# Kernel tuning notes

Measured on AMD Instinct MI355X. Metric: run time of the kernel, lower is better.

Reference implementation:

```python
import jax, jax.numpy as jnp
import numpy as np

N_NODES = 100000
N_EDGES = 1600000
D = 128
BN_EPS = 1e-5

def setup_inputs() -> dict:
    key = jax.random.key(0)
    ks = jax.random.split(key, 6)
    h = jax.random.normal(ks[0], (N_NODES, D), dtype=jnp.float32)
    src = jax.random.randint(ks[1], (N_EDGES,), 0, N_NODES, dtype=jnp.int32)
    dst = jax.random.randint(ks[2], (N_EDGES,), 0, N_NODES, dtype=jnp.int32)
    eps = jnp.zeros((1,), dtype=jnp.float32)
    # 2-layer GIN apply_func MLP, scaled for stable activations
    W1 = jax.random.normal(ks[3], (D, D), dtype=jnp.float32) / np.sqrt(D)
    b1 = jnp.zeros((D,), dtype=jnp.float32)
    W2 = jax.random.normal(ks[4], (D, D), dtype=jnp.float32) / np.sqrt(D)
    b2 = jnp.zeros((D,), dtype=jnp.float32)
    gamma = jnp.ones((D,), dtype=jnp.float32)
    beta = jnp.zeros((D,), dtype=jnp.float32)
    return {"h": h, "src": src, "dst": dst, "eps": eps,
            "W1": W1, "b1": b1, "W2": W2, "b2": b2,
            "gamma": gamma, "beta": beta}

def reference(h, src, dst, eps, W1, b1, W2, b2, gamma, beta):
    # --- neighbor sum aggregation: update_all(copy_u('h'), fn.sum) ---
    msgs = h[src]                                   # [E, D] irregular gather
    neigh = jax.ops.segment_sum(msgs, dst, num_segments=N_NODES)  # [N, D]
    # --- eps-scaled self term ---
    x = (1.0 + eps[0]) * h + neigh                  # [N, D]
    # --- apply_func: 2-layer MLP ---
    x = jax.nn.relu(x @ W1 + b1)
    x = x @ W2 + b2
    # --- BatchNorm1d over node dim (training-mode batch stats) ---
    mean = jnp.mean(x, axis=0)
    var = jnp.mean(jnp.square(x - mean), axis=0)
    x = (x - mean) * jax.lax.rsqrt(var + BN_EPS) * gamma + beta
    # --- activation + residual ---
    x = jax.nn.relu(x)
    x = h + x  # residual (in_dim == out_dim)
    return x
```

## Files before the change

### kernel.cpp

```cpp
#include <hip/hip_runtime.h>

#define NN 100000
#define NE 1600000
#define DD 128
#define BN_EPS 1e-5f

#define WSH 6
#define WSZ 64
#define NWIN ((NN + WSZ - 1) / WSZ)
#define NWINP 2048
#define EPB 8192
#define NBLK ((NE + EPB - 1) / EPB)
#define CAP 1536
#define PREPBLKS 828
#define GRID_PS (NBLK + PREPBLKS)
#define BN_BLOCKS 1024

typedef __attribute__((ext_vector_type(8))) short short8;
typedef __attribute__((ext_vector_type(4))) float floatx4;

__device__ __forceinline__ unsigned short f2bf(float f) {
    union { float f; unsigned u; } v; v.f = f;
    return (unsigned short)((v.u + 0x7FFFu + ((v.u >> 16) & 1u)) >> 16);
}
__device__ __forceinline__ float bf2f(unsigned short u) {
    union { unsigned u; float f; } v; v.u = ((unsigned)u) << 16;
    return v.f;
}

__global__ __launch_bounds__(256) void prep_scatter_kernel(
    float* __restrict__ stats,
    const float* __restrict__ W1, const float* __restrict__ W2,
    unsigned short* __restrict__ W1t, unsigned short* __restrict__ W2t,
    const float* __restrict__ h, unsigned short* __restrict__ hb, int do_hb,
    const int* __restrict__ src, const int* __restrict__ dst,
    int* __restrict__ wcnt, int* __restrict__ estage)
{
    __shared__ int lofs[NWINP];
    __shared__ int lcur[NWINP];
    __shared__ int gbase[NWINP];
    __shared__ int sorted[EPB];
    __shared__ int stmp[256];
    int t = threadIdx.x;

    if (blockIdx.x < NBLK) {
        int blk = blockIdx.x;
        for (int w = t; w < NWINP; w += 256) lcur[w] = 0;
        __syncthreads();
        int base = blk * EPB;
        int cnt = min(EPB, NE - base);
        for (int i = t; i < cnt; i += 256)
            atomicAdd(&lcur[dst[base + i] >> WSH], 1);
        __syncthreads();

        int w0 = t * 8;
        int c[8];
        int tsum = 0;
#pragma unroll
        for (int j = 0; j < 8; ++j) { c[j] = lcur[w0 + j]; tsum += c[j]; }
        stmp[t] = tsum;
        __syncthreads();
#pragma unroll
        for (int ofs = 1; ofs < 256; ofs <<= 1) {
            int u = (t >= ofs) ? stmp[t - ofs] : 0;
            __syncthreads();
            stmp[t] += u;
            __syncthreads();
        }
        int excl = stmp[t] - tsum;
#pragma unroll
        for (int j = 0; j < 8; ++j) {
            int w = w0 + j;
            lofs[w] = excl;
            lcur[w] = excl;
            int gb = (w < NWIN && c[j]) ? atomicAdd(&wcnt[w], c[j]) : 0;
            gbase[w] = w * CAP + gb;
            excl += c[j];
        }
        __syncthreads();

        for (int i = t; i < cnt; i += 256) {
            int d = dst[base + i];
            int s = src[base + i];
            int p = atomicAdd(&lcur[d >> WSH], 1);
            sorted[p] = (s << WSH) | (d & (WSZ - 1));
        }
        __syncthreads();

        for (int w = t; w < NWIN; w += 256) {
            int lb = lofs[w], le = lcur[w];
            int g = gbase[w];
            for (int j = lb; j < le; ++j)
                estage[g + (j - lb)] = sorted[j];
        }
    } else {
        int tid0 = (blockIdx.x - NBLK) * 256 + t;
        int stride = PREPBLKS * 256;
        if (tid0 < 2 * DD) stats[tid0] = 0.0f;
        for (int i = tid0; i < DD * DD; i += stride) {
            int n = i >> 7, k = i & 127;
            W1t[i] = f2bf(W1[k * DD + n]);
            W2t[i] = f2bf(W2[k * DD + n]);
        }
        if (do_hb) {
            const float4* h4 = (const float4*)h;
            ushort4* hb4 = (ushort4*)hb;
            for (int i = tid0; i < NN * (DD / 4); i += stride) {
                float4 v = h4[i];
                ushort4 o;
                o.x = f2bf(v.x); o.y = f2bf(v.y); o.z = f2bf(v.z); o.w = f2bf(v.w);
                hb4[i] = o;
            }
        }
    }
}

template <bool HB>
__global__ __launch_bounds__(256) void permgather_mlp_kernel(
    const float* __restrict__ h, const unsigned short* __restrict__ hb,
    const float* __restrict__ eps, const int* __restrict__ wcnt,
    const int* __restrict__ estage,
    const unsigned short* __restrict__ W1t, const unsigned short* __restrict__ W2t,
    const float* __restrict__ b1, const float* __restrict__ b2,
    unsigned short* __restrict__ Y, float* __restrict__ stats)
{
    __shared__ __align__(16) unsigned short xl[WSZ * 136];
    __shared__ __align__(16) char un[17408];

    int* es   = (int*)un;
    int* cnt  = (int*)(un + 6144);
    int* beg  = (int*)(un + 6144 + 256);
    int* cur  = (int*)(un + 6144 + 512);
    int* dh   = (int*)(un + 6144 + 768);
    int* dcur = (int*)(un + 6144 + 1024);
    unsigned char* order = (unsigned char*)(un + 6144 + 1280);
    unsigned short* wl = (unsigned short*)un;
    float* sred = (float*)un;
    float* qred = sred + 2048;

    const int b = blockIdx.x;
    const int t = threadIdx.x;
    const int lane = t & 63;
    const int wv = t >> 6;
    const int m = lane & 15;
    const int hi = lane >> 4;

    if (t < 64) { cnt[t] = 0; dh[t] = 0; }
    __syncthreads();
    int n = min(wcnt[b], CAP);
    int wbase = b * CAP;
    for (int i = t; i < n; i += 256)
        atomicAdd(&cnt[estage[wbase + i] & (WSZ - 1)], 1);
    __syncthreads();
    if (t < 64) beg[t] = cnt[t];
    __syncthreads();
#pragma unroll
    for (int ofs = 1; ofs < 64; ofs <<= 1) {
        int u = (t < 64 && t >= ofs) ? beg[t - ofs] : 0;
        __syncthreads();
        if (t < 64) beg[t] += u;
        __syncthreads();
    }
    if (t < 64) {
        int ex = beg[t] - cnt[t];
        beg[t] = ex;
        cur[t] = ex;
        atomicAdd(&dh[min(cnt[t], 63)], 1);
    }
    __syncthreads();
    if (t < 64) dcur[t] = dh[t];
    __syncthreads();
#pragma unroll
    for (int ofs = 1; ofs < 64; ofs <<= 1) {
        int u = (t < 64 && t >= ofs) ? dcur[t - ofs] : 0;
        __syncthreads();
        if (t < 64) dcur[t] += u;
        __syncthreads();
    }
    if (t < 64) dcur[t] -= dh[t];
    __syncthreads();
    if (t < 64) {
        int p = atomicAdd(&dcur[min(cnt[t], 63)], 1);
        order[p] = (unsigned char)t;
    }
    __syncthreads();
    for (int i = t; i < n; i += 256) {
        int e = estage[wbase + i];
        int p = atomicAdd(&cur[e & (WSZ - 1)], 1);
        es[p] = e >> WSH;
    }
    __syncthreads();

    const float sE = 1.0f + eps[0];
    const float4* h4 = (const float4*)h;
    const short8* hb8 = (const short8*)hb;
    const int c8 = t & 15;
#pragma unroll
    for (int pass = 0; pass < 4; ++pass) {
        int nl = order[pass * 16 + (t >> 4)];
        int node = b * WSZ + nl;
        if (node >= NN) {
            short8 z = {0, 0, 0, 0, 0, 0, 0, 0};
            *(short8*)&xl[nl * 136 + c8 * 8] = z;
            continue;
        }
        float4 a0 = h4[node * 32 + c8 * 2];
        float4 a1 = h4[node * 32 + c8 * 2 + 1];
        float acc[8] = {sE * a0.x, sE * a0.y, sE * a0.z, sE * a0.w,
                        sE * a1.x, sE * a1.y, sE * a1.z, sE * a1.w};
        int e = beg[nl], eend = beg[nl] + cnt[nl];
        if (HB) {
            for (; e + 3 < eend; e += 4) {
                int s0 = es[e], s1 = es[e + 1], s2 = es[e + 2], s3 = es[e + 3];
                short8 v0 = hb8[s0 * 16 + c8];
                short8 v1 = hb8[s1 * 16 + c8];
                short8 v2 = hb8[s2 * 16 + c8];
                short8 v3 = hb8[s3 * 16 + c8];
#pragma unroll
                for (int j = 0; j < 8; ++j) {
                    float t0 = bf2f((unsigned short)v0[j]) + bf2f((unsigned short)v1[j]);
                    float t1 = bf2f((unsigned short)v2[j]) + bf2f((unsigned short)v3[j]);
                    acc[j] += t0 + t1;
                }
            }
            for (; e < eend; ++e) {
                short8 v0 = hb8[es[e] * 16 + c8];
#pragma unroll
                for (int j = 0; j < 8; ++j) acc[j] += bf2f((unsigned short)v0[j]);
            }
        } else {
            for (; e + 1 < eend; e += 2) {
                int s0 = es[e], s1 = es[e + 1];
                float4 u0 = h4[s0 * 32 + c8 * 2], u1 = h4[s0 * 32 + c8 * 2 + 1];
                float4 w0 = h4[s1 * 32 + c8 * 2], w1 = h4[s1 * 32 + c8 * 2 + 1];
                acc[0] += u0.x + w0.x; acc[1] += u0.y + w0.y;
                acc[2] += u0.z + w0.z; acc[3] += u0.w + w0.w;
                acc[4] += u1.x + w1.x; acc[5] += u1.y + w1.y;
                acc[6] += u1.z + w1.z; acc[7] += u1.w + w1.w;
            }
            if (e < eend) {
                int s0 = es[e];
                float4 u0 = h4[s0 * 32 + c8 * 2], u1 = h4[s0 * 32 + c8 * 2 + 1];
                acc[0] += u0.x; acc[1] += u0.y; acc[2] += u0.z; acc[3] += u0.w;
                acc[4] += u1.x; acc[5] += u1.y; acc[6] += u1.z; acc[7] += u1.w;
            }
        }
        short8 o;
#pragma unroll
        for (int j = 0; j < 8; ++j) o[j] = (short)f2bf(acc[j]);
        *(short8*)&xl[nl * 136 + c8 * 8] = o;
    }
    __syncthreads();

    floatx4 acc[8];
#pragma unroll
    for (int i = 0; i < 8; ++i) acc[i] = (floatx4){0.f, 0.f, 0.f, 0.f};
    const short8* W1t8 = (const short8*)W1t;
#pragma unroll
    for (int hh = 0; hh < 2; ++hh) {
#pragma unroll
        for (int l = 0; l < 4; ++l) {
            int idx = t + l * 256;
            int nr = idx >> 4, c = idx & 15;
            *(short8*)&wl[nr * 136 + c * 8] = W1t8[(hh * 64 + nr) * 16 + c];
        }
        __syncthreads();
#pragma unroll
        for (int kc = 0; kc < 4; ++kc) {
            short8 a = *(const short8*)&xl[(wv * 16 + m) * 136 + kc * 32 + hi * 8];
#pragma unroll
            for (int ntl = 0; ntl < 4; ++ntl) {
                short8 bb = *(const short8*)&wl[(ntl * 16 + m) * 136 + kc * 32 + hi * 8];
                acc[hh * 4 + ntl] =
                    __builtin_amdgcn_mfma_f32_16x16x32_bf16(a, bb, acc[hh * 4 + ntl], 0, 0, 0);
            }
        }
        __syncthreads();
    }
#pragma unroll
    for (int nt = 0; nt < 8; ++nt) {
        float bv = b1[nt * 16 + m];
#pragma unroll
        for (int r = 0; r < 4; ++r) {
            float v = fmaxf(acc[nt][r] + bv, 0.f);
            xl[(wv * 16 + hi * 4 + r) * 136 + nt * 16 + m] = f2bf(v);
        }
    }
    __syncthreads();

#pragma unroll
    for (int i = 0; i < 8; ++i) acc[i] = (floatx4){0.f, 0.f, 0.f, 0.f};
    const short8* W2t8 = (const short8*)W2t;
#pragma unroll
    for (int hh = 0; hh < 2; ++hh) {
#pragma unroll
        for (int l = 0; l < 4; ++l) {
            int idx = t + l * 256;
            int nr = idx >> 4, c = idx & 15;
            *(short8*)&wl[nr * 136 + c * 8] = W2t8[(hh * 64 + nr) * 16 + c];
        }
        __syncthreads();
#pragma unroll
        for (int kc = 0; kc < 4; ++kc) {
            short8 a = *(const short8*)&xl[(wv * 16 + m) * 136 + kc * 32 + hi * 8];
#pragma unroll
            for (int ntl = 0; ntl < 4; ++ntl) {
                short8 bb = *(const short8*)&wl[(ntl * 16 + m) * 136 + kc * 32 + hi * 8];
                acc[hh * 4 + ntl] =
                    __builtin_amdgcn_mfma_f32_16x16x32_bf16(a, bb, acc[hh * 4 + ntl], 0, 0, 0);
            }
        }
        __syncthreads();
    }

#pragma unroll
    for (int nt = 0; nt < 8; ++nt) {
        float bv = b2[nt * 16 + m];
        float ss = 0.f, qq = 0.f;
#pragma unroll
        for (int r = 0; r < 4; ++r) {
            int row = wv * 16 + hi * 4 + r;
            float v = acc[nt][r] + bv;
            xl[row * 136 + nt * 16 + m] = f2bf(v);
            if (b * WSZ + row < NN) { ss += v; qq += v * v; }
        }
        sred[(nt * 16 + m) * 16 + wv * 4 + hi] = ss;
        qred[(nt * 16 + m) * 16 + wv * 4 + hi] = qq;
    }
    __syncthreads();

#pragma unroll
    for (int l = 0; l < 4; ++l) {
        int idx = t + l * 256;
        int row = idx >> 4, c = idx & 15;
        int g = b * WSZ + row;
        if (g < NN)
            ((short8*)Y)[g * 16 + c] = *(const short8*)&xl[row * 136 + c * 8];
    }
    if (t < 128) {
        float s = 0.f, q = 0.f;
#pragma unroll
        for (int j = 0; j < 16; ++j) { s += sred[t * 16 + j]; q += qred[t * 16 + j]; }
        atomicAdd(&stats[t], s);
        atomicAdd(&stats[DD + t], q);
    }
}

__global__ __launch_bounds__(256) void bn_final_kernel(
    const unsigned short* __restrict__ Y, const float* __restrict__ h,
    const float* __restrict__ gamma, const float* __restrict__ beta,
    const float* __restrict__ stats, float* __restrict__ out)
{
    const float invN = 1.0f / (float)NN;
    int t0 = blockIdx.x * 256 + threadIdx.x;
    int c8 = t0 & 15;
    float sc[8], sh[8];
#pragma unroll
    for (int j = 0; j < 8; ++j) {
        int col = c8 * 8 + j;
        float mu = stats[col] * invN;
        float var = stats[DD + col] * invN - mu * mu;
        float s = rsqrtf(var + BN_EPS) * gamma[col];
        sc[j] = s;
        sh[j] = beta[col] - mu * s;
    }
    const short8* Y8 = (const short8*)Y;
    const float4* H4 = (const float4*)h;
    float4* O4 = (float4*)out;
    const int total = NN * 16;
    const int stride = BN_BLOCKS * 256;
    for (int i = t0; i < total; i += stride) {
        short8 u = Y8[i];
        float4 h0 = H4[2 * i], h1 = H4[2 * i + 1];
        float4 r0, r1;
        r0.x = h0.x + fmaxf(bf2f((unsigned short)u[0]) * sc[0] + sh[0], 0.f);
        r0.y = h0.y + fmaxf(bf2f((unsigned short)u[1]) * sc[1] + sh[1], 0.f);
        r0.z = h0.z + fmaxf(bf2f((unsigned short)u[2]) * sc[2] + sh[2], 0.f);
        r0.w = h0.w + fmaxf(bf2f((unsigned short)u[3]) * sc[3] + sh[3], 0.f);
        r1.x = h1.x + fmaxf(bf2f((unsigned short)u[4]) * sc[4] + sh[4], 0.f);
        r1.y = h1.y + fmaxf(bf2f((unsigned short)u[5]) * sc[5] + sh[5], 0.f);
        r1.z = h1.z + fmaxf(bf2f((unsigned short)u[6]) * sc[6] + sh[6], 0.f);
        r1.w = h1.w + fmaxf(bf2f((unsigned short)u[7]) * sc[7] + sh[7], 0.f);
        O4[2 * i] = r0;
        O4[2 * i + 1] = r1;
    }
}

extern "C" void kernel_launch(void* const* d_in, const int* in_sizes, int n_in,
                              void* d_out, int out_size, void* d_ws, size_t ws_size,
                              hipStream_t stream)
{
    const float* h     = (const float*)d_in[0];
    const int*   src   = (const int*)d_in[1];
    const int*   dst   = (const int*)d_in[2];
    const float* eps   = (const float*)d_in[3];
    const float* W1    = (const float*)d_in[4];
    const float* b1    = (const float*)d_in[5];
    const float* W2    = (const float*)d_in[6];
    const float* b2    = (const float*)d_in[7];
    const float* gamma = (const float*)d_in[8];
    const float* beta  = (const float*)d_in[9];
    float* out = (float*)d_out;

    char* w = (char*)d_ws;
    size_t o = 0;
    float* stats    = (float*)(w + o); o += 256 * 4;
    int* wcnt       = (int*)(w + o); o += NWINP * 4;
    unsigned short* W1t = (unsigned short*)(w + o); o += (size_t)DD * DD * 2;
    unsigned short* W2t = (unsigned short*)(w + o); o += (size_t)DD * DD * 2;
    int* estage     = (int*)(w + o); o += (size_t)NWIN * CAP * 4;
    unsigned short* xb  = (unsigned short*)(w + o); o += (size_t)NN * DD * 2;
    unsigned short* hb  = (unsigned short*)(w + o); o += (size_t)NN * DD * 2;
    const int use_hb = (ws_size >= o) ? 1 : 0;

    hipMemsetAsync(wcnt, 0, NWINP * sizeof(int), stream);

    prep_scatter_kernel<<<GRID_PS, 256, 0, stream>>>(
        stats, W1, W2, W1t, W2t, h, hb, use_hb, src, dst, wcnt, estage);

    if (use_hb)
        permgather_mlp_kernel<true><<<NWIN, 256, 0, stream>>>(
            h, hb, eps, wcnt, estage, W1t, W2t, b1, b2, xb, stats);
    else
        permgather_mlp_kernel<false><<<NWIN, 256, 0, stream>>>(
            h, hb, eps, wcnt, estage, W1t, W2t, b1, b2, xb, stats);

    bn_final_kernel<<<BN_BLOCKS, 256, 0, stream>>>(xb, h, gamma, beta, stats, out);
}
```

Before: 287.1 us.

## Fuse prep, gather-MLP and BN into one cooperative persistent kernel

Replaces the memset plus three kernel launches with a single cooperative kernel that uses grid-wide syncs between the phases: zeroing, edge scatter and weight conversion, windowed gather plus MLP, then BN finalisation. The edge scatter drops the shared-memory local sort and writes each edge straight to global memory through atomically advanced per-window cursors. Windows are now processed by a persistent grid of at most 1024 blocks, capped by occupancy. This removes launch gaps and one staging pass, at the cost of grid-barrier overhead, less parallelism in the scatter and MLP phases, and less coalesced scatter writes.

```diff
diff --git a/kernel.cpp b/kernel.cpp
--- a/kernel.cpp
+++ b/kernel.cpp
@@ -1,4 +1,7 @@
 #include <hip/hip_runtime.h>
+#include <hip/hip_cooperative_groups.h>
+
+namespace cg = cooperative_groups;
 
 #define NN 100000
 #define NE 1600000
@@ -10,11 +13,9 @@
 #define NWIN ((NN + WSZ - 1) / WSZ)
 #define NWINP 2048
 #define EPB 8192
-#define NBLK ((NE + EPB - 1) / EPB)
+#define NSCAT ((NE + EPB - 1) / EPB)
 #define CAP 1536
-#define PREPBLKS 828
-#define GRID_PS (NBLK + PREPBLKS)
-#define BN_BLOCKS 1024
+#define MAXGRID 1024
 
 typedef __attribute__((ext_vector_type(8))) short short8;
 typedef __attribute__((ext_vector_type(4))) float floatx4;
@@ -28,83 +29,79 @@
     return v.f;
 }
 
-__global__ __launch_bounds__(256) void prep_scatter_kernel(
-    float* __restrict__ stats,
-    const float* __restrict__ W1, const float* __restrict__ W2,
-    unsigned short* __restrict__ W1t, unsigned short* __restrict__ W2t,
-    const float* __restrict__ h, unsigned short* __restrict__ hb, int do_hb,
-    const int* __restrict__ src, const int* __restrict__ dst,
-    int* __restrict__ wcnt, int* __restrict__ estage)
+struct GinParams {
+    const float* h; const int* src; const int* dst; const float* eps;
+    const float* W1; const float* b1; const float* W2; const float* b2;
+    const float* gamma; const float* beta;
+    float* out;
+    float* stats; int* wcnt;
+    unsigned short* W1t; unsigned short* W2t;
+    int* estage; unsigned short* xb; unsigned short* hb;
+};
+
+template <bool HB>
+__global__ __launch_bounds__(256, 4) void gin_mega_kernel(GinParams p)
 {
-    __shared__ int lofs[NWINP];
-    __shared__ int lcur[NWINP];
-    __shared__ int gbase[NWINP];
-    __shared__ int sorted[EPB];
-    __shared__ int stmp[256];
-    int t = threadIdx.x;
-
-    if (blockIdx.x < NBLK) {
-        int blk = blockIdx.x;
-        for (int w = t; w < NWINP; w += 256) lcur[w] = 0;
-        __syncthreads();
-        int base = blk * EPB;
-        int cnt = min(EPB, NE - base);
-        for (int i = t; i < cnt; i += 256)
-            atomicAdd(&lcur[dst[base + i] >> WSH], 1);
-        __syncthreads();
-
-        int w0 = t * 8;
-        int c[8];
-        int tsum = 0;
-#pragma unroll
-        for (int j = 0; j < 8; ++j) { c[j] = lcur[w0 + j]; tsum += c[j]; }
-        stmp[t] = tsum;
-        __syncthreads();
-#pragma unroll
-        for (int ofs = 1; ofs < 256; ofs <<= 1) {
-            int u = (t >= ofs) ? stmp[t - ofs] : 0;
-            __syncthreads();
-            stmp[t] += u;
-            __syncthreads();
-        }
-        int excl = stmp[t] - tsum;
-#pragma unroll
-        for (int j = 0; j < 8; ++j) {
-            int w = w0 + j;
-            lofs[w] = excl;
-            lcur[w] = excl;
-            int gb = (w < NWIN && c[j]) ? atomicAdd(&wcnt[w], c[j]) : 0;
-            gbase[w] = w * CAP + gb;
-            excl += c[j];
-        }
-        __syncthreads();
-
-        for (int i = t; i < cnt; i += 256) {
-            int d = dst[base + i];
-            int s = src[base + i];
-            int p = atomicAdd(&lcur[d >> WSH], 1);
-            sorted[p] = (s << WSH) | (d & (WSZ - 1));
-        }
-        __syncthreads();
-
+    __shared__ __align__(16) char smem[34816];
+    unsigned short* xl = (unsigned short*)smem;
+    char* un = smem + 17408;
+    int* bins = (int*)smem;
+
+    int* es   = (int*)un;
+    int* cnt  = (int*)(un + 6144);
+    int* beg  = (int*)(un + 6400);
+    int* cur  = (int*)(un + 6656);
+    int* dh   = (int*)(un + 6912);
+    int* dcur = (int*)(un + 7168);
+    unsigned char* order = (unsigned char*)(un + 7424);
+    unsigned short* wl = (unsigned short*)un;
+    float* sred = (float*)un;
+    float* qred = sred + 2048;
+
+    cg::grid_group grid = cg::this_grid();
+    const int t = threadIdx.x;
+    const int bid = blockIdx.x;
+    const int nb = gridDim.x;
+    const int lane = t & 63;
+    const int wv = t >> 6;
+    const int m = lane & 15;
+    const int hi = lane >> 4;
+
+    int gi = bid * 256 + t;
+    if (gi < NWINP) p.wcnt[gi] = 0;
+    if (gi < 2 * DD) p.stats[gi] = 0.0f;
+    grid.sync();
+
+    if (bid < NSCAT) {
+        for (int w = t; w < NWINP; w += 256) bins[w] = 0;
+        __syncthreads();
+        int base = bid * EPB;
+        int ecnt = min(EPB, NE - base);
+        for (int i = t; i < ecnt; i += 256)
+            atomicAdd(&bins[p.dst[base + i] >> WSH], 1);
+        __syncthreads();
         for (int w = t; w < NWIN; w += 256) {
-            int lb = lofs[w], le = lcur[w];
-            int g = gbase[w];
-            for (int j = lb; j < le; ++j)
-                estage[g + (j - lb)] = sorted[j];
+            int c = bins[w];
+            int gb = c ? atomicAdd(&p.wcnt[w], c) : 0;
+            bins[w] = w * CAP + gb;
+        }
+        __syncthreads();
+        for (int i = t; i < ecnt; i += 256) {
+            int d = p.dst[base + i];
+            int pos = atomicAdd(&bins[d >> WSH], 1);
+            p.estage[pos] = (p.src[base + i] << WSH) | (d & (WSZ - 1));
         }
     } else {
-        int tid0 = (blockIdx.x - NBLK) * 256 + t;
-        int stride = PREPBLKS * 256;
-        if (tid0 < 2 * DD) stats[tid0] = 0.0f;
+        int tid0 = (bid - NSCAT) * 256 + t;
+        int stride = (nb - NSCAT) * 256;
         for (int i = tid0; i < DD * DD; i += stride) {
             int n = i >> 7, k = i & 127;
-            W1t[i] = f2bf(W1[k * DD + n]);
-            W2t[i] = f2bf(W2[k * DD + n]);
-        }
-        if (do_hb) {
-            const float4* h4 = (const float4*)h;
-            ushort4* hb4 = (ushort4*)hb;
+            p.W1t[i] = f2bf(p.W1[k * DD + n]);
+            p.W2t[i] = f2bf(p.W2[k * DD + n]);
+        }
+        if (HB) {
+            const float4* h4 = (const float4*)p.h;
+            ushort4* hb4 = (ushort4*)p.hb;
             for (int i = tid0; i < NN * (DD / 4); i += stride) {
                 float4 v = h4[i];
                 ushort4 o;
@@ -113,276 +110,247 @@
             }
         }
     }
-}
-
-template <bool HB>
-__global__ __launch_bounds__(256) void permgather_mlp_kernel(
-    const float* __restrict__ h, const unsigned short* __restrict__ hb,
-    const float* __restrict__ eps, const int* __restrict__ wcnt,
-    const int* __restrict__ estage,
-    const unsigned short* __restrict__ W1t, const unsigned short* __restrict__ W2t,
-    const float* __restrict__ b1, const float* __restrict__ b2,
-    unsigned short* __restrict__ Y, float* __restrict__ stats)
-{
-    __shared__ __align__(16) unsigned short xl[WSZ * 136];
-    __shared__ __align__(16) char un[17408];
-
-    int* es   = (int*)un;
-    int* cnt  = (int*)(un + 6144);
-    int* beg  = (int*)(un + 6144 + 256);
-    int* cur  = (int*)(un + 6144 + 512);
-    int* dh   = (int*)(un + 6144 + 768);
-    int* dcur = (int*)(un + 6144 + 1024);
-    unsigned char* order = (unsigned char*)(un + 6144 + 1280);
-    unsigned short* wl = (unsigned short*)un;
-    float* sred = (float*)un;
-    float* qred = sred + 2048;
-
-    const int b = blockIdx.x;
-    const int t = threadIdx.x;
-    const int lane = t & 63;
-    const int wv = t >> 6;
-    const int m = lane & 15;
-    const int hi = lane >> 4;
-
-    if (t < 64) { cnt[t] = 0; dh[t] = 0; }
-    __syncthreads();
-    int n = min(wcnt[b], CAP);
-    int wbase = b * CAP;
-    for (int i = t; i < n; i += 256)
-        atomicAdd(&cnt[estage[wbase + i] & (WSZ - 1)], 1);
-    __syncthreads();
-    if (t < 64) beg[t] = cnt[t];
-    __syncthreads();
-#pragma unroll
-    for (int ofs = 1; ofs < 64; ofs <<= 1) {
-        int u = (t < 64 && t >= ofs) ? beg[t - ofs] : 0;
-        __syncthreads();
-        if (t < 64) beg[t] += u;
-        __syncthreads();
-    }
-    if (t < 64) {
-        int ex = beg[t] - cnt[t];
-        beg[t] = ex;
-        cur[t] = ex;
-        atomicAdd(&dh[min(cnt[t], 63)], 1);
-    }
-    __syncthreads();
-    if (t < 64) dcur[t] = dh[t];
-    __syncthreads();
-#pragma unroll
-    for (int ofs = 1; ofs < 64; ofs <<= 1) {
-        int u = (t < 64 && t >= ofs) ? dcur[t - ofs] : 0;
-        __syncthreads();
-        if (t < 64) dcur[t] += u;
-        __syncthreads();
-    }
-    if (t < 64) dcur[t] -= dh[t];
-    __syncthreads();
-    if (t < 64) {
-        int p = atomicAdd(&dcur[min(cnt[t], 63)], 1);
-        order[p] = (unsigned char)t;
-    }
-    __syncthreads();
-    for (int i = t; i < n; i += 256) {
-        int e = estage[wbase + i];
-        int p = atomicAdd(&cur[e & (WSZ - 1)], 1);
-        es[p] = e >> WSH;
-    }
-    __syncthreads();
-
-    const float sE = 1.0f + eps[0];
-    const float4* h4 = (const float4*)h;
-    const short8* hb8 = (const short8*)hb;
+    grid.sync();
+
+    const float sE = 1.0f + p.eps[0];
+    const float4* h4 = (const float4*)p.h;
+    const short8* hb8 = (const short8*)p.hb;
     const int c8 = t & 15;
-#pragma unroll
-    for (int pass = 0; pass < 4; ++pass) {
-        int nl = order[pass * 16 + (t >> 4)];
-        int node = b * WSZ + nl;
-        if (node >= NN) {
-            short8 z = {0, 0, 0, 0, 0, 0, 0, 0};
-            *(short8*)&xl[nl * 136 + c8 * 8] = z;
-            continue;
-        }
-        float4 a0 = h4[node * 32 + c8 * 2];
-        float4 a1 = h4[node * 32 + c8 * 2 + 1];
-        float acc[8] = {sE * a0.x, sE * a0.y, sE * a0.z, sE * a0.w,
-                        sE * a1.x, sE * a1.y, sE * a1.z, sE * a1.w};
-        int e = beg[nl], eend = beg[nl] + cnt[nl];
-        if (HB) {
-            for (; e + 3 < eend; e += 4) {
-                int s0 = es[e], s1 = es[e + 1], s2 = es[e + 2], s3 = es[e + 3];
-                short8 v0 = hb8[s0 * 16 + c8];
-                short8 v1 = hb8[s1 * 16 + c8];
-                short8 v2 = hb8[s2 * 16 + c8];
-                short8 v3 = hb8[s3 * 16 + c8];
-#pragma unroll
-                for (int j = 0; j < 8; ++j) {
-                    float t0 = bf2f((unsigned short)v0[j]) + bf2f((unsigned short)v1[j]);
-                    float t1 = bf2f((unsigned short)v2[j]) + bf2f((unsigned short)v3[j]);
-                    acc[j] += t0 + t1;
-                }
-            }
-            for (; e < eend; ++e) {
-                short8 v0 = hb8[es[e] * 16 + c8];
-#pragma unroll
-                for (int j = 0; j < 8; ++j) acc[j] += bf2f((unsigned short)v0[j]);
-            }
-        } else {
-            for (; e + 1 < eend; e += 2) {
-                int s0 = es[e], s1 = es[e + 1];
-                float4 u0 = h4[s0 * 32 + c8 * 2], u1 = h4[s0 * 32 + c8 * 2 + 1];
-                float4 w0 = h4[s1 * 32 + c8 * 2], w1 = h4[s1 * 32 + c8 * 2 + 1];
-                acc[0] += u0.x + w0.x; acc[1] += u0.y + w0.y;
-                acc[2] += u0.z + w0.z; acc[3] += u0.w + w0.w;
-                acc[4] += u1.x + w1.x; acc[5] += u1.y + w1.y;
-                acc[6] += u1.z + w1.z; acc[7] += u1.w + w1.w;
-            }
-            if (e < eend) {
-                int s0 = es[e];
-                float4 u0 = h4[s0 * 32 + c8 * 2], u1 = h4[s0 * 32 + c8 * 2 + 1];
-                acc[0] += u0.x; acc[1] += u0.y; acc[2] += u0.z; acc[3] += u0.w;
-                acc[4] += u1.x; acc[5] += u1.y; acc[6] += u1.z; acc[7] += u1.w;
-            }
-        }
-        short8 o;
-#pragma unroll
-        for (int j = 0; j < 8; ++j) o[j] = (short)f2bf(acc[j]);
-        *(short8*)&xl[nl * 136 + c8 * 8] = o;
-    }
-    __syncthreads();
-
-    floatx4 acc[8];
-#pragma unroll
-    for (int i = 0; i < 8; ++i) acc[i] = (floatx4){0.f, 0.f, 0.f, 0.f};
-    const short8* W1t8 = (const short8*)W1t;
-#pragma unroll
-    for (int hh = 0; hh < 2; ++hh) {
+
+    for (int wdx = bid; wdx < NWIN; wdx += nb) {
+        __syncthreads();
+        if (t < 64) { cnt[t] = 0; dh[t] = 0; }
+        __syncthreads();
+        int n = min(p.wcnt[wdx], CAP);
+        int wbase = wdx * CAP;
+        for (int i = t; i < n; i += 256)
+            atomicAdd(&cnt[p.estage[wbase + i] & (WSZ - 1)], 1);
+        __syncthreads();
+        if (t < 64) beg[t] = cnt[t];
+        __syncthreads();
+#pragma unroll
+        for (int ofs = 1; ofs < 64; ofs <<= 1) {
+            int u = (t < 64 && t >= ofs) ? beg[t - ofs] : 0;
+            __syncthreads();
+            if (t < 64) beg[t] += u;
+            __syncthreads();
+        }
+        if (t < 64) {
+            int ex = beg[t] - cnt[t];
+            beg[t] = ex;
+            cur[t] = ex;
+            atomicAdd(&dh[min(cnt[t], 63)], 1);
+        }
+        __syncthreads();
+        if (t < 64) dcur[t] = dh[t];
+        __syncthreads();
+#pragma unroll
+        for (int ofs = 1; ofs < 64; ofs <<= 1) {
+            int u = (t < 64 && t >= ofs) ? dcur[t - ofs] : 0;
+            __syncthreads();
+            if (t < 64) dcur[t] += u;
+            __syncthreads();
+        }
+        if (t < 64) dcur[t] -= dh[t];
+        __syncthreads();
+        if (t < 64) {
+            int pp = atomicAdd(&dcur[min(cnt[t], 63)], 1);
+            order[pp] = (unsigned char)t;
+        }
+        __syncthreads();
+        for (int i = t; i < n; i += 256) {
+            int e = p.estage[wbase + i];
+            int pp = atomicAdd(&cur[e & (WSZ - 1)], 1);
+            es[pp] = e >> WSH;
+        }
+        __syncthreads();
+
+#pragma unroll
+        for (int pass = 0; pass < 4; ++pass) {
+            int nl = order[pass * 16 + (t >> 4)];
+            int node = wdx * WSZ + nl;
+            if (node >= NN) {
+                short8 z = {0, 0, 0, 0, 0, 0, 0, 0};
+                *(short8*)&xl[nl * 136 + c8 * 8] = z;
+                continue;
+            }
+            float4 a0 = h4[node * 32 + c8 * 2];
+            float4 a1 = h4[node * 32 + c8 * 2 + 1];
+            float acc[8] = {sE * a0.x, sE * a0.y, sE * a0.z, sE * a0.w,
+                            sE * a1.x, sE * a1.y, sE * a1.z, sE * a1.w};
+            int e = beg[nl], eend = beg[nl] + cnt[nl];
+            if (HB) {
+                for (; e + 3 < eend; e += 4) {
+                    int s0 = es[e], s1 = es[e + 1], s2 = es[e + 2], s3 = es[e + 3];
+                    short8 v0 = hb8[s0 * 16 + c8];
+                    short8 v1 = hb8[s1 * 16 + c8];
+                    short8 v2 = hb8[s2 * 16 + c8];
+                    short8 v3 = hb8[s3 * 16 + c8];
+#pragma unroll
+                    for (int j = 0; j < 8; ++j) {
+                        float t0 = bf2f((unsigned short)v0[j]) + bf2f((unsigned short)v1[j]);
+                        float t1 = bf2f((unsigned short)v2[j]) + bf2f((unsigned short)v3[j]);
+                        acc[j] += t0 + t1;
+                    }
+                }
+                for (; e < eend; ++e) {
+                    short8 v0 = hb8[es[e] * 16 + c8];
+#pragma unroll
+                    for (int j = 0; j < 8; ++j) acc[j] += bf2f((unsigned short)v0[j]);
+                }
+            } else {
+                for (; e + 1 < eend; e += 2) {
+                    int s0 = es[e], s1 = es[e + 1];
+                    float4 u0 = h4[s0 * 32 + c8 * 2], u1 = h4[s0 * 32 + c8 * 2 + 1];
+                    float4 w0 = h4[s1 * 32 + c8 * 2], w1 = h4[s1 * 32 + c8 * 2 + 1];
+                    acc[0] += u0.x + w0.x; acc[1] += u0.y + w0.y;
+                    acc[2] += u0.z + w0.z; acc[3] += u0.w + w0.w;
+                    acc[4] += u1.x + w1.x; acc[5] += u1.y + w1.y;
+                    acc[6] += u1.z + w1.z; acc[7] += u1.w + w1.w;
+                }
+                if (e < eend) {
+                    int s0 = es[e];
+                    float4 u0 = h4[s0 * 32 + c8 * 2], u1 = h4[s0 * 32 + c8 * 2 + 1];
+                    acc[0] += u0.x; acc[1] += u0.y; acc[2] += u0.z; acc[3] += u0.w;
+                    acc[4] += u1.x; acc[5] += u1.y; acc[6] += u1.z; acc[7] += u1.w;
+                }
+            }
+            short8 o;
+#pragma unroll
+            for (int j = 0; j < 8; ++j) o[j] = (short)f2bf(acc[j]);
+            *(short8*)&xl[nl * 136 + c8 * 8] = o;
+        }
+        __syncthreads();
+
+        floatx4 acc[8];
+#pragma unroll
+        for (int i = 0; i < 8; ++i) acc[i] = (floatx4){0.f, 0.f, 0.f, 0.f};
+        const short8* W1t8 = (const short8*)p.W1t;
+#pragma unroll
+        for (int hh = 0; hh < 2; ++hh) {
+#pragma unroll
+            for (int l = 0; l < 4; ++l) {
+                int idx = t + l * 256;
+                int nr = idx >> 4, c = idx & 15;
+                *(short8*)&wl[nr * 136 + c * 8] = W1t8[(hh * 64 + nr) * 16 + c];
+            }
+            __syncthreads();
+#pragma unroll
+            for (int kc = 0; kc < 4; ++kc) {
+                short8 a = *(const short8*)&xl[(wv * 16 + m) * 136 + kc * 32 + hi * 8];
+#pragma unroll
+                for (int ntl = 0; ntl < 4; ++ntl) {
+                    short8 bb = *(const short8*)&wl[(ntl * 16 + m) * 136 + kc * 32 + hi * 8];
+                    acc[hh * 4 + ntl] =
+                        __builtin_amdgcn_mfma_f32_16x16x32_bf16(a, bb, acc[hh * 4 + ntl], 0, 0, 0);
+                }
+            }
+            __syncthreads();
+        }
+#pragma unroll
+        for (int nt = 0; nt < 8; ++nt) {
+            float bv = p.b1[nt * 16 + m];
+#pragma unroll
+            for (int r = 0; r < 4; ++r) {
+                float v = fmaxf(acc[nt][r] + bv, 0.f);
+                xl[(wv * 16 + hi * 4 + r) * 136 + nt * 16 + m] = f2bf(v);
+            }
+        }
+        __syncthreads();
+
+#pragma unroll
+        for (int i = 0; i < 8; ++i) acc[i] = (floatx4){0.f, 0.f, 0.f, 0.f};
+        const short8* W2t8 = (const short8*)p.W2t;
+#pragma unroll
+        for (int hh = 0; hh < 2; ++hh) {
+#pragma unroll
+            for (int l = 0; l < 4; ++l) {
+                int idx = t + l * 256;
+                int nr = idx >> 4, c = idx & 15;
+                *(short8*)&wl[nr * 136 + c * 8] = W2t8[(hh * 64 + nr) * 16 + c];
+            }
+            __syncthreads();
+#pragma unroll
+            for (int kc = 0; kc < 4; ++kc) {
+                short8 a = *(const short8*)&xl[(wv * 16 + m) * 136 + kc * 32 + hi * 8];
+#pragma unroll
+                for (int ntl = 0; ntl < 4; ++ntl) {
+                    short8 bb = *(const short8*)&wl[(ntl * 16 + m) * 136 + kc * 32 + hi * 8];
+                    acc[hh * 4 + ntl] =
+                        __builtin_amdgcn_mfma_f32_16x16x32_bf16(a, bb, acc[hh * 4 + ntl], 0, 0, 0);
+                }
+            }
+            __syncthreads();
+        }
+
+#pragma unroll
+        for (int nt = 0; nt < 8; ++nt) {
+            float bv = p.b2[nt * 16 + m];
+            float ss = 0.f, qq = 0.f;
+#pragma unroll
+            for (int r = 0; r < 4; ++r) {
+                int row = wv * 16 + hi * 4 + r;
+                float v = acc[nt][r] + bv;
+                xl[row * 136 + nt * 16 + m] = f2bf(v);
+                if (wdx * WSZ + row < NN) { ss += v; qq += v * v; }
+            }
+            sred[(nt * 16 + m) * 16 + wv * 4 + hi] = ss;
+            qred[(nt * 16 + m) * 16 + wv * 4 + hi] = qq;
+        }
+        __syncthreads();
+
 #pragma unroll
         for (int l = 0; l < 4; ++l) {
             int idx = t + l * 256;
-            int nr = idx >> 4, c = idx & 15;
-            *(short8*)&wl[nr * 136 + c * 8] = W1t8[(hh * 64 + nr) * 16 + c];
-        }
-        __syncthreads();
-#pragma unroll
-        for (int kc = 0; kc < 4; ++kc) {
-            short8 a = *(const short8*)&xl[(wv * 16 + m) * 136 + kc * 32 + hi * 8];
-#pragma unroll
-            for (int ntl = 0; ntl < 4; ++ntl) {
-                short8 bb = *(const short8*)&wl[(ntl * 16 + m) * 136 + kc * 32 + hi * 8];
-                acc[hh * 4 + ntl] =
-                    __builtin_amdgcn_mfma_f32_16x16x32_bf16(a, bb, acc[hh * 4 + ntl], 0, 0, 0);
-            }
-        }
-        __syncthreads();
+            int row = idx >> 4, c = idx & 15;
+            int g = wdx * WSZ + row;
+            if (g < NN)
+                ((short8*)p.xb)[g * 16 + c] = *(const short8*)&xl[row * 136 + c * 8];
+        }
+        if (t < 128) {
+            float s = 0.f, q = 0.f;
+#pragma unroll
+            for (int j = 0; j < 16; ++j) { s += sred[t * 16 + j]; q += qred[t * 16 + j]; }
+            atomicAdd(&p.stats[t], s);
+            atomicAdd(&p.stats[DD + t], q);
+        }
     }
-#pragma unroll
-    for (int nt = 0; nt < 8; ++nt) {
-        float bv = b1[nt * 16 + m];
-#pragma unroll
-        for (int r = 0; r < 4; ++r) {
-            float v = fmaxf(acc[nt][r] + bv, 0.f);
-            xl[(wv * 16 + hi * 4 + r) * 136 + nt * 16 + m] = f2bf(v);
-        }
-    }
-    __syncthreads();
-
-#pragma unroll
-    for (int i = 0; i < 8; ++i) acc[i] = (floatx4){0.f, 0.f, 0.f, 0.f};
-    const short8* W2t8 = (const short8*)W2t;
-#pragma unroll
-    for (int hh = 0; hh < 2; ++hh) {
-#pragma unroll
-        for (int l = 0; l < 4; ++l) {
-            int idx = t + l * 256;
-            int nr = idx >> 4, c = idx & 15;
-            *(short8*)&wl[nr * 136 + c * 8] = W2t8[(hh * 64 + nr) * 16 + c];
-        }
-        __syncthreads();
-#pragma unroll
-        for (int kc = 0; kc < 4; ++kc) {
-            short8 a = *(const short8*)&xl[(wv * 16 + m) * 136 + kc * 32 + hi * 8];
-#pragma unroll
-            for (int ntl = 0; ntl < 4; ++ntl) {
-                short8 bb = *(const short8*)&wl[(ntl * 16 + m) * 136 + kc * 32 + hi * 8];
-                acc[hh * 4 + ntl] =
-                    __builtin_amdgcn_mfma_f32_16x16x32_bf16(a, bb, acc[hh * 4 + ntl], 0, 0, 0);
-            }
-        }
-        __syncthreads();
-    }
-
-#pragma unroll
-    for (int nt = 0; nt < 8; ++nt) {
-        float bv = b2[nt * 16 + m];
-        float ss = 0.f, qq = 0.f;
-#pragma unroll
-        for (int r = 0; r < 4; ++r) {
-            int row = wv * 16 + hi * 4 + r;
-            float v = acc[nt][r] + bv;
-            xl[row * 136 + nt * 16 + m] = f2bf(v);
-            if (b * WSZ + row < NN) { ss += v; qq += v * v; }
-        }
-        sred[(nt * 16 + m) * 16 + wv * 4 + hi] = ss;
-        qred[(nt * 16 + m) * 16 + wv * 4 + hi] = qq;
-    }
-    __syncthreads();
-
-#pragma unroll
-    for (int l = 0; l < 4; ++l) {
-        int idx = t + l * 256;
-        int row = idx >> 4, c = idx & 15;
-        int g = b * WSZ + row;
-        if (g < NN)
-            ((short8*)Y)[g * 16 + c] = *(const short8*)&xl[row * 136 + c * 8];
-    }
-    if (t < 128) {
-        float s = 0.f, q = 0.f;
-#pragma unroll
-        for (int j = 0; j < 16; ++j) { s += sred[t * 16 + j]; q += qred[t * 16 + j]; }
-        atomicAdd(&stats[t], s);
-        atomicAdd(&stats[DD + t], q);
-    }
-}
-
-__global__ __launch_bounds__(256) void bn_final_kernel(
-    const unsigned short* __restrict__ Y, const float* __restrict__ h,
-    const float* __restrict__ gamma, const float* __restrict__ beta,
-    const float* __restrict__ stats, float* __restrict__ out)
-{
-    const float invN = 1.0f / (float)NN;
-    int t0 = blockIdx.x * 256 + threadIdx.x;
-    int c8 = t0 & 15;
-    float sc[8], sh[8];
-#pragma unroll
-    for (int j = 0; j < 8; ++j) {
-        int col = c8 * 8 + j;
-        float mu = stats[col] * invN;
-        float var = stats[DD + col] * invN - mu * mu;
-        float s = rsqrtf(var + BN_EPS) * gamma[col];
-        sc[j] = s;
-        sh[j] = beta[col] - mu * s;
-    }
-    const short8* Y8 = (const short8*)Y;
-    const float4* H4 = (const float4*)h;
-    float4* O4 = (float4*)out;
-    const int total = NN * 16;
-    const int stride = BN_BLOCKS * 256;
-    for (int i = t0; i < total; i += stride) {
-        short8 u = Y8[i];
-        float4 h0 = H4[2 * i], h1 = H4[2 * i + 1];
-        float4 r0, r1;
-        r0.x = h0.x + fmaxf(bf2f((unsigned short)u[0]) * sc[0] + sh[0], 0.f);
-        r0.y = h0.y + fmaxf(bf2f((unsigned short)u[1]) * sc[1] + sh[1], 0.f);
-        r0.z = h0.z + fmaxf(bf2f((unsigned short)u[2]) * sc[2] + sh[2], 0.f);
-        r0.w = h0.w + fmaxf(bf2f((unsigned short)u[3]) * sc[3] + sh[3], 0.f);
-        r1.x = h1.x + fmaxf(bf2f((unsigned short)u[4]) * sc[4] + sh[4], 0.f);
-        r1.y = h1.y + fmaxf(bf2f((unsigned short)u[5]) * sc[5] + sh[5], 0.f);
-        r1.z = h1.z + fmaxf(bf2f((unsigned short)u[6]) * sc[6] + sh[6], 0.f);
-        r1.w = h1.w + fmaxf(bf2f((unsigned short)u[7]) * sc[7] + sh[7], 0.f);
-        O4[2 * i] = r0;
-        O4[2 * i + 1] = r1;
+    grid.sync();
+
+    {
+        const float invN = 1.0f / (float)NN;
+        int t0 = bid * 256 + t;
+        int cc = t0 & 15;
+        float sc[8], sh[8];
+#pragma unroll
+        for (int j = 0; j < 8; ++j) {
+            int col = cc * 8 + j;
+            float mu = p.stats[col] * invN;
+            float var = p.stats[DD + col] * invN - mu * mu;
+            float s = rsqrtf(var + BN_EPS) * p.gamma[col];
+            sc[j] = s;
+            sh[j] = p.beta[col] - mu * s;
+        }
+        const short8* Y8 = (const short8*)p.xb;
+        const float4* H4 = (const float4*)p.h;
+        float4* O4 = (float4*)p.out;
+        const int total = NN * 16;
+        const int stride = nb * 256;
+        for (int i = t0; i < total; i += stride) {
+            short8 u = Y8[i];
+            float4 h0 = H4[2 * i], h1 = H4[2 * i + 1];
+            float4 r0, r1;
+            r0.x = h0.x + fmaxf(bf2f((unsigned short)u[0]) * sc[0] + sh[0], 0.f);
+            r0.y = h0.y + fmaxf(bf2f((unsigned short)u[1]) * sc[1] + sh[1], 0.f);
+            r0.z = h0.z + fmaxf(bf2f((unsigned short)u[2]) * sc[2] + sh[2], 0.f);
+            r0.w = h0.w + fmaxf(bf2f((unsigned short)u[3]) * sc[3] + sh[3], 0.f);
+            r1.x = h1.x + fmaxf(bf2f((unsigned short)u[4]) * sc[4] + sh[4], 0.f);
+            r1.y = h1.y + fmaxf(bf2f((unsigned short)u[5]) * sc[5] + sh[5], 0.f);
+            r1.z = h1.z + fmaxf(bf2f((unsigned short)u[6]) * sc[6] + sh[6], 0.f);
+            r1.w = h1.w + fmaxf(bf2f((unsigned short)u[7]) * sc[7] + sh[7], 0.f);
+            O4[2 * i] = r0;
+            O4[2 * i + 1] = r1;
+        }
     }
 }
 
@@ -390,40 +358,45 @@
                               void* d_out, int out_size, void* d_ws, size_t ws_size,
                               hipStream_t stream)
 {
-    const float* h     = (const float*)d_in[0];
-    const int*   src   = (const int*)d_in[1];
-    const int*   dst   = (const int*)d_in[2];
-    const float* eps   = (const float*)d_in[3];
-    const float* W1    = (const float*)d_in[4];
-    const float* b1    = (const float*)d_in[5];
-    const float* W2    = (const float*)d_in[6];
-    const float* b2    = (const float*)d_in[7];
-    const float* gamma = (const float*)d_in[8];
-    const float* beta  = (const float*)d_in[9];
-    float* out = (float*)d_out;
+    GinParams prm;
+    prm.h     = (const float*)d_in[0];
+    prm.src   = (const int*)d_in[1];
+    prm.dst   = (const int*)d_in[2];
+    prm.eps   = (const float*)d_in[3];
+    prm.W1    = (const float*)d_in[4];
+    prm.b1    = (const float*)d_in[5];
+    prm.W2    = (const float*)d_in[6];
+    prm.b2    = (const float*)d_in[7];
+    prm.gamma = (const float*)d_in[8];
+    prm.beta  = (const float*)d_in[9];
+    prm.out   = (float*)d_out;
 
     char* w = (char*)d_ws;
     size_t o = 0;
-    float* stats    = (float*)(w + o); o += 256 * 4;
-    int* wcnt       = (int*)(w + o); o += NWINP * 4;
-    unsigned short* W1t = (unsigned short*)(w + o); o += (size_t)DD * DD * 2;
-    unsigned short* W2t = (unsigned short*)(w + o); o += (size_t)DD * DD * 2;
-    int* estage     = (int*)(w + o); o += (size_t)NWIN * CAP * 4;
-    unsigned short* xb  = (unsigned short*)(w + o); o += (size_t)NN * DD * 2;
-    unsigned short* hb  = (unsigned short*)(w + o); o += (size_t)NN * DD * 2;
+    prm.stats  = (float*)(w + o); o += 256 * 4;
+    prm.wcnt   = (int*)(w + o); o += NWINP * 4;
+    prm.W1t    = (unsigned short*)(w + o); o += (size_t)DD * DD * 2;
+    prm.W2t    = (unsigned short*)(w + o); o += (size_t)DD * DD * 2;
+    prm.estage = (int*)(w + o); o += (size_t)NWIN * CAP * 4;
+    prm.xb     = (unsigned short*)(w + o); o += (size_t)NN * DD * 2;
+    prm.hb     = (unsigned short*)(w + o); o += (size_t)NN * DD * 2;
     const int use_hb = (ws_size >= o) ? 1 : 0;
 
-    hipMemsetAsync(wcnt, 0, NWINP * sizeof(int), stream);
-
-    prep_scatter_kernel<<<GRID_PS, 256, 0, stream>>>(
-        stats, W1, W2, W1t, W2t, h, hb, use_hb, src, dst, wcnt, estage);
-
+    int maxb = 0;
     if (use_hb)
-        permgather_mlp_kernel<true><<<NWIN, 256, 0, stream>>>(
-            h, hb, eps, wcnt, estage, W1t, W2t, b1, b2, xb, stats);
+        hipOccupancyMaxActiveBlocksPerMultiprocessor(&maxb, gin_mega_kernel<true>, 256, 0);
     else
-        permgather_mlp_kernel<false><<<NWIN, 256, 0, stream>>>(
-            h, hb, eps, wcnt, estage, W1t, W2t, b1, b2, xb, stats);
-
-    bn_final_kernel<<<BN_BLOCKS, 256, 0, stream>>>(xb, h, gamma, beta, stats, out);
+        hipOccupancyMaxActiveBlocksPerMultiprocessor(&maxb, gin_mega_kernel<false>, 256, 0);
+    if (maxb <= 0) maxb = 4;
+    int grid = maxb * 256;
+    if (grid > MAXGRID) grid = MAXGRID;
+    if (grid < 256) grid = 256;
+
+    void* kargs[] = { &prm };
+    if (use_hb)
+        hipLaunchCooperativeKernel(reinterpret_cast<void*>(gin_mega_kernel<true>),
+                                   dim3(grid), dim3(256), kargs, 0, stream);
+    else
+        hipLaunchCooperativeKernel(reinterpret_cast<void*>(gin_mega_kernel<false>),
+                                   dim3(grid), dim3(256), kargs, 0, stream);
 }
```

Measured after the change: 496.0 us. 72.8% more time.

## Bucket edges into 512-node superbins and sort per node in a separate permute kernel

Applied to the files above, without the earlier changes.

The edge bucketing now bins by 512-node superbins (196 bins) instead of 64-node windows (1563 bins). This cuts the shared-memory footprint and the global atomic contention in the scatter kernel, and gives longer contiguous write runs. A new permute kernel sorts each superbin by destination node in place and writes per-node begin/end offsets. The gather/MLP kernel then reads source indices straight from global memory instead of doing its own per-window counting sort in shared memory. The cost is an extra kernel launch, an extra pass over the edge buffer, and source-index loads that now come from global memory rather than LDS.

```diff
diff --git a/kernel.cpp b/kernel.cpp
--- a/kernel.cpp
+++ b/kernel.cpp
@@ -5,15 +5,16 @@
 #define DD 128
 #define BN_EPS 1e-5f
 
-#define WSH 6
-#define WSZ 64
-#define NWIN ((NN + WSZ - 1) / WSZ)
-#define NWINP 2048
+#define SBSH 9
+#define SBSZ 512
+#define NSB ((NN + SBSZ - 1) / SBSZ)
+#define CAPS 9216
 #define EPB 8192
 #define NBLK ((NE + EPB - 1) / EPB)
-#define CAP 1536
 #define PREPBLKS 828
 #define GRID_PS (NBLK + PREPBLKS)
+#define TSZ 64
+#define NTILE ((NN + TSZ - 1) / TSZ)
 #define BN_BLOCKS 1024
 
 typedef __attribute__((ext_vector_type(8))) short short8;
@@ -29,36 +30,29 @@
 }
 
 __global__ __launch_bounds__(256) void prep_scatter_kernel(
-    float* __restrict__ stats,
     const float* __restrict__ W1, const float* __restrict__ W2,
     unsigned short* __restrict__ W1t, unsigned short* __restrict__ W2t,
     const float* __restrict__ h, unsigned short* __restrict__ hb, int do_hb,
     const int* __restrict__ src, const int* __restrict__ dst,
-    int* __restrict__ wcnt, int* __restrict__ estage)
+    int* __restrict__ scnt, int* __restrict__ sbuf)
 {
-    __shared__ int lofs[NWINP];
-    __shared__ int lcur[NWINP];
-    __shared__ int gbase[NWINP];
+    __shared__ int bins[256];
+    __shared__ int lofs[256];
+    __shared__ int gbase[256];
+    __shared__ int stmp[256];
     __shared__ int sorted[EPB];
-    __shared__ int stmp[256];
     int t = threadIdx.x;
 
     if (blockIdx.x < NBLK) {
-        int blk = blockIdx.x;
-        for (int w = t; w < NWINP; w += 256) lcur[w] = 0;
-        __syncthreads();
-        int base = blk * EPB;
-        int cnt = min(EPB, NE - base);
-        for (int i = t; i < cnt; i += 256)
-            atomicAdd(&lcur[dst[base + i] >> WSH], 1);
-        __syncthreads();
-
-        int w0 = t * 8;
-        int c[8];
-        int tsum = 0;
-#pragma unroll
-        for (int j = 0; j < 8; ++j) { c[j] = lcur[w0 + j]; tsum += c[j]; }
-        stmp[t] = tsum;
+        bins[t] = 0;
+        __syncthreads();
+        int base = blockIdx.x * EPB;
+        int ecnt = min(EPB, NE - base);
+        for (int i = t; i < ecnt; i += 256)
+            atomicAdd(&bins[dst[base + i] >> SBSH], 1);
+        __syncthreads();
+        int c = bins[t];
+        stmp[t] = c;
         __syncthreads();
 #pragma unroll
         for (int ofs = 1; ofs < 256; ofs <<= 1) {
@@ -67,36 +61,29 @@
             stmp[t] += u;
             __syncthreads();
         }
-        int excl = stmp[t] - tsum;
-#pragma unroll
-        for (int j = 0; j < 8; ++j) {
-            int w = w0 + j;
-            lofs[w] = excl;
-            lcur[w] = excl;
-            int gb = (w < NWIN && c[j]) ? atomicAdd(&wcnt[w], c[j]) : 0;
-            gbase[w] = w * CAP + gb;
-            excl += c[j];
-        }
-        __syncthreads();
-
-        for (int i = t; i < cnt; i += 256) {
+        int excl = stmp[t] - c;
+        lofs[t] = excl;
+        int gb = (t < NSB && c) ? atomicAdd(&scnt[t], c) : 0;
+        gbase[t] = t * CAPS + gb;
+        bins[t] = excl;
+        __syncthreads();
+
+        for (int i = t; i < ecnt; i += 256) {
             int d = dst[base + i];
-            int s = src[base + i];
-            int p = atomicAdd(&lcur[d >> WSH], 1);
-            sorted[p] = (s << WSH) | (d & (WSZ - 1));
-        }
-        __syncthreads();
-
-        for (int w = t; w < NWIN; w += 256) {
-            int lb = lofs[w], le = lcur[w];
-            int g = gbase[w];
+            int p = atomicAdd(&bins[d >> SBSH], 1);
+            sorted[p] = (src[base + i] << SBSH) | (d & (SBSZ - 1));
+        }
+        __syncthreads();
+
+        for (int sb = t; sb < NSB; sb += 256) {
+            int lb = lofs[sb], le = bins[sb];
+            int g = gbase[sb];
             for (int j = lb; j < le; ++j)
-                estage[g + (j - lb)] = sorted[j];
+                sbuf[g + (j - lb)] = sorted[j];
         }
     } else {
         int tid0 = (blockIdx.x - NBLK) * 256 + t;
         int stride = PREPBLKS * 256;
-        if (tid0 < 2 * DD) stats[tid0] = 0.0f;
         for (int i = tid0; i < DD * DD; i += stride) {
             int n = i >> 7, k = i & 127;
             W1t[i] = f2bf(W1[k * DD + n]);
@@ -115,25 +102,65 @@
     }
 }
 
+__global__ __launch_bounds__(512) void permute_kernel(
+    const int* __restrict__ scnt, int* __restrict__ sbuf,
+    int2* __restrict__ off2)
+{
+    __shared__ int ew[CAPS];
+    __shared__ int cnt[SBSZ];
+    __shared__ int beg[SBSZ];
+    __shared__ int cur[SBSZ];
+    __shared__ int stmp[512];
+    int sb = blockIdx.x, t = threadIdx.x;
+    cnt[t] = 0;
+    __syncthreads();
+    int n = min(scnt[sb], CAPS);
+    int sbase = sb * CAPS;
+    for (int i = t; i < n; i += 512) {
+        int e = sbuf[sbase + i];
+        ew[i] = e;
+        atomicAdd(&cnt[e & (SBSZ - 1)], 1);
+    }
+    __syncthreads();
+    int c = cnt[t];
+    stmp[t] = c;
+    __syncthreads();
+#pragma unroll
+    for (int ofs = 1; ofs < 512; ofs <<= 1) {
+        int u = (t >= ofs) ? stmp[t - ofs] : 0;
+        __syncthreads();
+        stmp[t] += u;
+        __syncthreads();
+    }
+    int excl = stmp[t] - c;
+    beg[t] = excl;
+    cur[t] = excl;
+    off2[sb * SBSZ + t] = make_int2(sbase + excl, sbase + excl + c);
+    __syncthreads();
+    for (int i = t; i < n; i += 512) {
+        int e = ew[i];
+        int p = atomicAdd(&cur[e & (SBSZ - 1)], 1);
+        sbuf[sbase + p] = e >> SBSH;
+    }
+}
+
 template <bool HB>
-__global__ __launch_bounds__(256) void permgather_mlp_kernel(
+__global__ __launch_bounds__(256) void gather_mlp_kernel(
     const float* __restrict__ h, const unsigned short* __restrict__ hb,
-    const float* __restrict__ eps, const int* __restrict__ wcnt,
-    const int* __restrict__ estage,
+    const float* __restrict__ eps, const int2* __restrict__ off2,
+    const int* __restrict__ srcs,
     const unsigned short* __restrict__ W1t, const unsigned short* __restrict__ W2t,
     const float* __restrict__ b1, const float* __restrict__ b2,
     unsigned short* __restrict__ Y, float* __restrict__ stats)
 {
-    __shared__ __align__(16) unsigned short xl[WSZ * 136];
+    __shared__ __align__(16) unsigned short xl[TSZ * 136];
     __shared__ __align__(16) char un[17408];
 
-    int* es   = (int*)un;
-    int* cnt  = (int*)(un + 6144);
-    int* beg  = (int*)(un + 6144 + 256);
-    int* cur  = (int*)(un + 6144 + 512);
-    int* dh   = (int*)(un + 6144 + 768);
-    int* dcur = (int*)(un + 6144 + 1024);
-    unsigned char* order = (unsigned char*)(un + 6144 + 1280);
+    int* beg64 = (int*)un;
+    int* cnt64 = (int*)(un + 256);
+    int* dh    = (int*)(un + 512);
+    int* dcur  = (int*)(un + 768);
+    unsigned char* order = (unsigned char*)(un + 1024);
     unsigned short* wl = (unsigned short*)un;
     float* sred = (float*)un;
     float* qred = sred + 2048;
@@ -145,27 +172,13 @@
     const int m = lane & 15;
     const int hi = lane >> 4;
 
-    if (t < 64) { cnt[t] = 0; dh[t] = 0; }
-    __syncthreads();
-    int n = min(wcnt[b], CAP);
-    int wbase = b * CAP;
-    for (int i = t; i < n; i += 256)
-        atomicAdd(&cnt[estage[wbase + i] & (WSZ - 1)], 1);
-    __syncthreads();
-    if (t < 64) beg[t] = cnt[t];
-    __syncthreads();
-#pragma unroll
-    for (int ofs = 1; ofs < 64; ofs <<= 1) {
-        int u = (t < 64 && t >= ofs) ? beg[t - ofs] : 0;
-        __syncthreads();
-        if (t < 64) beg[t] += u;
-        __syncthreads();
-    }
+    if (t < 64) dh[t] = 0;
+    __syncthreads();
     if (t < 64) {
-        int ex = beg[t] - cnt[t];
-        beg[t] = ex;
-        cur[t] = ex;
-        atomicAdd(&dh[min(cnt[t], 63)], 1);
+        int2 oo = off2[b * TSZ + t];
+        beg64[t] = oo.x;
+        cnt64[t] = oo.y - oo.x;
+        atomicAdd(&dh[min(cnt64[t], 63)], 1);
     }
     __syncthreads();
     if (t < 64) dcur[t] = dh[t];
@@ -180,14 +193,8 @@
     if (t < 64) dcur[t] -= dh[t];
     __syncthreads();
     if (t < 64) {
-        int p = atomicAdd(&dcur[min(cnt[t], 63)], 1);
+        int p = atomicAdd(&dcur[min(cnt64[t], 63)], 1);
         order[p] = (unsigned char)t;
-    }
-    __syncthreads();
-    for (int i = t; i < n; i += 256) {
-        int e = estage[wbase + i];
-        int p = atomicAdd(&cur[e & (WSZ - 1)], 1);
-        es[p] = e >> WSH;
     }
     __syncthreads();
 
@@ -198,7 +205,7 @@
 #pragma unroll
     for (int pass = 0; pass < 4; ++pass) {
         int nl = order[pass * 16 + (t >> 4)];
-        int node = b * WSZ + nl;
+        int node = b * TSZ + nl;
         if (node >= NN) {
             short8 z = {0, 0, 0, 0, 0, 0, 0, 0};
             *(short8*)&xl[nl * 136 + c8 * 8] = z;
@@ -208,10 +215,10 @@
         float4 a1 = h4[node * 32 + c8 * 2 + 1];
         float acc[8] = {sE * a0.x, sE * a0.y, sE * a0.z, sE * a0.w,
                         sE * a1.x, sE * a1.y, sE * a1.z, sE * a1.w};
-        int e = beg[nl], eend = beg[nl] + cnt[nl];
+        int e = beg64[nl], eend = beg64[nl] + cnt64[nl];
         if (HB) {
             for (; e + 3 < eend; e += 4) {
-                int s0 = es[e], s1 = es[e + 1], s2 = es[e + 2], s3 = es[e + 3];
+                int s0 = srcs[e], s1 = srcs[e + 1], s2 = srcs[e + 2], s3 = srcs[e + 3];
                 short8 v0 = hb8[s0 * 16 + c8];
                 short8 v1 = hb8[s1 * 16 + c8];
                 short8 v2 = hb8[s2 * 16 + c8];
@@ -224,13 +231,13 @@
                 }
             }
             for (; e < eend; ++e) {
-                short8 v0 = hb8[es[e] * 16 + c8];
+                short8 v0 = hb8[srcs[e] * 16 + c8];
 #pragma unroll
                 for (int j = 0; j < 8; ++j) acc[j] += bf2f((unsigned short)v0[j]);
             }
         } else {
             for (; e + 1 < eend; e += 2) {
-                int s0 = es[e], s1 = es[e + 1];
+                int s0 = srcs[e], s1 = srcs[e + 1];
                 float4 u0 = h4[s0 * 32 + c8 * 2], u1 = h4[s0 * 32 + c8 * 2 + 1];
                 float4 w0 = h4[s1 * 32 + c8 * 2], w1 = h4[s1 * 32 + c8 * 2 + 1];
                 acc[0] += u0.x + w0.x; acc[1] += u0.y + w0.y;
@@ -239,7 +246,7 @@
                 acc[6] += u1.z + w1.z; acc[7] += u1.w + w1.w;
             }
             if (e < eend) {
-                int s0 = es[e];
+                int s0 = srcs[e];
                 float4 u0 = h4[s0 * 32 + c8 * 2], u1 = h4[s0 * 32 + c8 * 2 + 1];
                 acc[0] += u0.x; acc[1] += u0.y; acc[2] += u0.z; acc[3] += u0.w;
                 acc[4] += u1.x; acc[5] += u1.y; acc[6] += u1.z; acc[7] += u1.w;
@@ -322,7 +329,7 @@
             int row = wv * 16 + hi * 4 + r;
             float v = acc[nt][r] + bv;
             xl[row * 136 + nt * 16 + m] = f2bf(v);
-            if (b * WSZ + row < NN) { ss += v; qq += v * v; }
+            if (b * TSZ + row < NN) { ss += v; qq += v * v; }
         }
         sred[(nt * 16 + m) * 16 + wv * 4 + hi] = ss;
         qred[(nt * 16 + m) * 16 + wv * 4 + hi] = qq;
@@ -333,7 +340,7 @@
     for (int l = 0; l < 4; ++l) {
         int idx = t + l * 256;
         int row = idx >> 4, c = idx & 15;
-        int g = b * WSZ + row;
+        int g = b * TSZ + row;
         if (g < NN)
             ((short8*)Y)[g * 16 + c] = *(const short8*)&xl[row * 136 + c * 8];
     }
@@ -405,25 +412,28 @@
     char* w = (char*)d_ws;
     size_t o = 0;
     float* stats    = (float*)(w + o); o += 256 * 4;
-    int* wcnt       = (int*)(w + o); o += NWINP * 4;
+    int* scnt       = (int*)(w + o); o += 256 * 4;
     unsigned short* W1t = (unsigned short*)(w + o); o += (size_t)DD * DD * 2;
     unsigned short* W2t = (unsigned short*)(w + o); o += (size_t)DD * DD * 2;
-    int* estage     = (int*)(w + o); o += (size_t)NWIN * CAP * 4;
+    int2* off2      = (int2*)(w + o); o += (size_t)NSB * SBSZ * 8;
+    int* sbuf       = (int*)(w + o); o += (size_t)NSB * CAPS * 4;
     unsigned short* xb  = (unsigned short*)(w + o); o += (size_t)NN * DD * 2;
     unsigned short* hb  = (unsigned short*)(w + o); o += (size_t)NN * DD * 2;
     const int use_hb = (ws_size >= o) ? 1 : 0;
 
-    hipMemsetAsync(wcnt, 0, NWINP * sizeof(int), stream);
+    hipMemsetAsync(stats, 0, 512 * sizeof(int), stream);
 
     prep_scatter_kernel<<<GRID_PS, 256, 0, stream>>>(
-        stats, W1, W2, W1t, W2t, h, hb, use_hb, src, dst, wcnt, estage);
+        W1, W2, W1t, W2t, h, hb, use_hb, src, dst, scnt, sbuf);
+
+    permute_kernel<<<NSB, 512, 0, stream>>>(scnt, sbuf, off2);
 
     if (use_hb)
-        permgather_mlp_kernel<true><<<NWIN, 256, 0, stream>>>(
-            h, hb, eps, wcnt, estage, W1t, W2t, b1, b2, xb, stats);
+        gather_mlp_kernel<true><<<NTILE, 256, 0, stream>>>(
+            h, hb, eps, off2, sbuf, W1t, W2t, b1, b2, xb, stats);
     else
-        permgather_mlp_kernel<false><<<NWIN, 256, 0, stream>>>(
-            h, hb, eps, wcnt, estage, W1t, W2t, b1, b2, xb, stats);
+        gather_mlp_kernel<false><<<NTILE, 256, 0, stream>>>(
+            h, hb, eps, off2, sbuf, W1t, W2t, b1, b2, xb, stats);
 
     bn_final_kernel<<<BN_BLOCKS, 256, 0, stream>>>(xb, h, gamma, beta, stats, out);
 }
```

Result: no change. 287.2 us (+0.1%).
